# Optimization experiments

Measured on AMD Instinct MI355X. Metric: run time of the kernel, lower is better.

Reference implementation:

```python
import jax, jax.numpy as jnp
import numpy as np

N_E = 8192
E_DIM = 255  # spatial dim; full Lorentz dim = E_DIM + 1
BETA = 0.25
EPS = 1e-7


def _rand_lorentz(key, n, d):
    """Sample n points on the Lorentz manifold (curvature c=1), radii in [1,6]."""
    k1, k2 = jax.random.split(key)
    radii = jax.random.uniform(k1, (n, 1)) * 5.0 + 1.0
    t = jnp.cosh(radii)  # time component, >= cosh(1)
    dirs = jax.random.normal(k2, (n, d))
    dirs = dirs / jnp.linalg.norm(dirs, axis=-1, keepdims=True)
    s = dirs * jnp.sqrt(jnp.maximum(t ** 2 - 1.0, 1e-7))
    return jnp.concatenate([t, s], axis=-1)


def setup_inputs() -> dict:
    key = jax.random.key(0)
    k_u, k_cb = jax.random.split(key)
    B, H, W = 8, 32, 32
    u = _rand_lorentz(k_u, B * H * W, E_DIM).reshape(B, H, W, E_DIM + 1)
    codebook = _rand_lorentz(k_cb, N_E, E_DIM)
    return {"u_hyp": u, "codebook": codebook}


def reference(u_hyp, codebook):
    shape = u_hyp.shape
    d_full = E_DIM + 1
    u = u_hyp.reshape(-1, d_full)          # [N, D]
    n = u.shape[0]
    # Minkowski metric signs: (-, +, +, ..., +)
    signs = jnp.concatenate([-jnp.ones((1,), u.dtype), jnp.ones((E_DIM,), u.dtype)])

    # Lorentzian inner products with all codes: <u, c>_L = -u0*c0 + u_s . c_s
    K = (u * signs) @ codebook.T           # [N, n_e]
    dist = jnp.arccosh(jnp.maximum(-K, 1.0 + EPS))  # hyperbolic distance (c=1)
    idx = jnp.argmin(dist, axis=-1)        # [N]
    x_q = codebook[idx]                    # [N, D] gather

    def pdist(a, b):  # elementwise Lorentzian distance
        inner = jnp.sum(a * b * signs, axis=-1)
        return jnp.arccosh(jnp.maximum(-inner, 1.0 + EPS))

    sg = jax.lax.stop_gradient
    codebook_loss = pdist(sg(u), x_q).mean()
    commitment_loss = pdist(u, sg(x_q)).mean()
    loss = codebook_loss + BETA * commitment_loss

    # straight-through estimator
    z_q = (u + sg(x_q - u)).reshape(shape)

    counts = jnp.zeros((N_E,), u.dtype).at[idx].add(1.0)
    e_mean = counts / n
    entropy = -jnp.sum(e_mean * jnp.log(e_mean + 1e-10))
    perplexity = jnp.exp(entropy)
    diversity_loss = entropy
    return loss, z_q, perplexity, diversity_loss, e_mean
```

## Files before the change

### kernel.cpp

```cpp
#include <hip/hip_runtime.h>
#include <hip/hip_bf16.h>
#include <stdint.h>

#define N_PTS   8192
#define D       256
#define N_E     8192
#define BETA    0.25f
#define EPS_1   1.0000001f

typedef unsigned long long u64;
typedef __attribute__((ext_vector_type(8))) short bf16x8;
typedef __attribute__((ext_vector_type(8))) short short8;
typedef __attribute__((ext_vector_type(4))) float f32x4;

#define WS_KEYS    0
#define WS_COUNTS  (N_PTS * 8)
#define WS_LOSS    (WS_COUNTS + N_E * 4)
#define WS_RB_DONE (WS_LOSS + 16)
#define WS_GDONE   (WS_RB_DONE + 64 * 4)
#define WS_AHI     (1 << 20)
#define WS_ALO     (WS_AHI + N_PTS * D * 2)
#define WS_BHI     (WS_ALO + N_PTS * D * 2)
#define WS_BLO     (WS_BHI + N_E * D * 2)

__device__ __forceinline__ short f2bf(float x) {
    __hip_bfloat16 h = __float2bfloat16(x);
    return *reinterpret_cast<short*>(&h);
}
__device__ __forceinline__ float bf2f(short s) {
    __hip_bfloat16 h = *reinterpret_cast<__hip_bfloat16*>(&s);
    return __bfloat162float(h);
}

#define GLOAD16(gp, lp) __builtin_amdgcn_global_load_lds(                      \
    (const __attribute__((address_space(1))) void*)(gp),                       \
    (__attribute__((address_space(3))) void*)(lp), 16, 0, 0)

#define DPP_MIN(x, ctrl)                                                       \
    x = fminf(x, __int_as_float(__builtin_amdgcn_update_dpp(                   \
            __float_as_int(x), __float_as_int(x), (ctrl), 0xF, 0xF, true)))

__global__ __launch_bounds__(256) void k_prep(
    const float* __restrict__ u, const float* __restrict__ cb,
    short* __restrict__ Ahi, short* __restrict__ Alo,
    short* __restrict__ Bhi, short* __restrict__ Blo,
    u64* __restrict__ keys, float* __restrict__ counts,
    double* __restrict__ loss_sum, unsigned* __restrict__ rb_done,
    unsigned* __restrict__ gdone)
{
    const int tid = blockIdx.x * 256 + threadIdx.x;
    if (tid < N_E)   counts[tid] = 0.f;
    if (tid < N_PTS) keys[tid] = ~0ULL;
    if (tid == 0)    *loss_sum = 0.0;
    if (tid < 64)    rb_done[tid] = 0u;
    if (tid == 64)   *gdone = 0u;

    const int blk = tid >> 6;
    const int l   = tid & 63;
    const int s   = blk >> 3, c = blk & 7;
    const int p   = s * 16 + (l & 15);
    const int k   = c * 32 + (l >> 4) * 8;
    const size_t gin  = (size_t)p * D + k;
    const size_t gout = (size_t)tid * 8;

    float v[8];
    short8 h8, l8;

    *(float4*)&v[0] = *(const float4*)&u[gin];
    *(float4*)&v[4] = *(const float4*)&u[gin + 4];
    if (k == 0) v[0] = -v[0];
    #pragma unroll
    for (int j = 0; j < 8; ++j) {
        h8[j] = f2bf(v[j]);
        l8[j] = f2bf(v[j] - bf2f(h8[j]));
    }
    *(short8*)&Ahi[gout] = h8;
    *(short8*)&Alo[gout] = l8;

    *(float4*)&v[0] = *(const float4*)&cb[gin];
    *(float4*)&v[4] = *(const float4*)&cb[gin + 4];
    #pragma unroll
    for (int j = 0; j < 8; ++j) {
        h8[j] = f2bf(v[j]);
        l8[j] = f2bf(v[j] - bf2f(h8[j]));
    }
    *(short8*)&Bhi[gout] = h8;
    *(short8*)&Blo[gout] = l8;
}

#define BMM 128
#define BNN 128
#define NKS (D / 32)

__global__ __launch_bounds__(256, 4) void k_argmin_mfma(
    const short* __restrict__ Ahi, const short* __restrict__ Alo,
    const short* __restrict__ Bhi, const short* __restrict__ Blo,
    u64* __restrict__ keys,
    const float* __restrict__ u, const float* __restrict__ cb,
    float* __restrict__ out, float* __restrict__ counts,
    double* __restrict__ loss_sum, unsigned* __restrict__ rb_done,
    unsigned* __restrict__ gdone)
{
    __shared__ short sm[4][8 * 512];

    const int t   = threadIdx.x;
    const int w   = t >> 6;
    const int l   = t & 63;
    const int rb  = blockIdx.x >> 6;
    const int cbk = blockIdx.x & 63;
    const int r0  = rb * BMM, c0 = cbk * BNN;
    const int wr  = w >> 1, wc = w & 1;

    const short* gsrc = (w == 0) ? Ahi : (w == 1) ? Alo : (w == 2) ? Bhi : Blo;
    short* ldst = sm[w];
    const int s0 = ((w < 2) ? rb : cbk) * 8;

    f32x4 acc[4][4];
    #pragma unroll
    for (int i = 0; i < 4; ++i)
        #pragma unroll
        for (int j = 0; j < 4; ++j) acc[i][j] = (f32x4){0.f, 0.f, 0.f, 0.f};

    for (int kk = 0; kk < NKS; ++kk) {
        __syncthreads();
        #pragma unroll
        for (int i = 0; i < 8; ++i)
            GLOAD16(gsrc + (size_t)((s0 + i) * 8 + kk) * 512 + l * 8,
                    ldst + i * 512);
        __syncthreads();

        bf16x8 ah[4], al[4], bh[4], bl[4];
        #pragma unroll
        for (int f = 0; f < 4; ++f) {
            ah[f] = *(const bf16x8*)&sm[0][(wr * 4 + f) * 512 + l * 8];
            al[f] = *(const bf16x8*)&sm[1][(wr * 4 + f) * 512 + l * 8];
            bh[f] = *(const bf16x8*)&sm[2][(wc * 4 + f) * 512 + l * 8];
            bl[f] = *(const bf16x8*)&sm[3][(wc * 4 + f) * 512 + l * 8];
        }
        #pragma unroll
        for (int mf = 0; mf < 4; ++mf)
            #pragma unroll
            for (int nf = 0; nf < 4; ++nf) {
                acc[mf][nf] = __builtin_amdgcn_mfma_f32_16x16x32_bf16(
                    ah[mf], bh[nf], acc[mf][nf], 0, 0, 0);
                acc[mf][nf] = __builtin_amdgcn_mfma_f32_16x16x32_bf16(
                    ah[mf], bl[nf], acc[mf][nf], 0, 0, 0);
                acc[mf][nf] = __builtin_amdgcn_mfma_f32_16x16x32_bf16(
                    al[mf], bh[nf], acc[mf][nf], 0, 0, 0);
            }
    }

    const int g  = l >> 4;
    const int cc = l & 15;
    #pragma unroll
    for (int mf = 0; mf < 4; ++mf) {
        #pragma unroll
        for (int r = 0; r < 4; ++r) {
            float mm = fmaxf(-acc[mf][0][r], EPS_1);
            unsigned code = (unsigned)(c0 + wc * 64 + cc);
            #pragma unroll
            for (int nf = 1; nf < 4; ++nf) {
                float mv = fmaxf(-acc[mf][nf][r], EPS_1);
                if (mv < mm) { mm = mv; code = (unsigned)(c0 + wc * 64 + nf * 16 + cc); }
            }
            float mv = mm;
            DPP_MIN(mv, 0xB1);
            DPP_MIN(mv, 0x4E);
            DPP_MIN(mv, 0x141);
            DPP_MIN(mv, 0x140);
            if (mm == mv) {
                const int row = r0 + wr * 64 + mf * 16 + g * 4 + r;
                u64 key = ((u64)__float_as_uint(mm) << 32) | code;
                atomicMin(&keys[row], key);
            }
        }
    }

    int* sflagp = (int*)&sm[3][0];
    __syncthreads();
    if (t == 0)
        *sflagp = (atomicAdd(&rb_done[rb], 1u) == 63u) ? 1 : 0;
    __syncthreads();
    if (!*sflagp) return;

    u64* smk = (u64*)&sm[0][0];
    if (t < BMM)
        smk[t] = atomicMin(&keys[r0 + t], ~0ULL);
    __syncthreads();

    float* zq = out + 1;
    float fsum = 0.f;
    for (int rr = 0; rr < 32; ++rr) {
        const int lrow = w * 32 + rr;
        const int row  = r0 + lrow;
        const int idx  = (int)(unsigned)(smk[lrow] & 0xffffffffULL);
        float4 uv = *(const float4*)&u[(size_t)row * D + l * 4];
        float4 cv = *(const float4*)&cb[(size_t)idx * D + l * 4];
        if (l == 0) uv.x = -uv.x;
        float partial = uv.x * cv.x + uv.y * cv.y + uv.z * cv.z + uv.w * cv.w;
        *(float4*)&zq[(size_t)row * D + l * 4] = cv;
        #pragma unroll
        for (int s = 32; s >= 1; s >>= 1)
            partial += __shfl_xor(partial, s);
        if (l == 0) {
            fsum += acoshf(fmaxf(-partial, EPS_1));
            atomicAdd(&counts[idx], 1.f);
        }
    }
    if (l == 0) atomicAdd(loss_sum, (double)fsum);

    __syncthreads();
    if (t == 0)
        *sflagp = (atomicAdd(gdone, 1u) == 63u) ? 1 : 0;
    __syncthreads();
    if (!*sflagp) return;

    float* red = (float*)&sm[1][0];
    const int OFF_P = 1 + N_PTS * D;
    float ent = 0.f;
    for (int i = t; i < N_E; i += 256) {
        float cv_ = atomicAdd(&counts[i], 0.f);
        float e = cv_ * (1.0f / N_PTS);
        out[OFF_P + 2 + i] = e;
        ent -= e * logf(e + 1e-10f);
    }
    red[t] = ent;
    __syncthreads();
    for (int s = 128; s > 0; s >>= 1) {
        if (t < s) red[t] += red[t + s];
        __syncthreads();
    }
    if (t == 0) {
        float entropy = red[0];
        double ls = atomicAdd(loss_sum, 0.0);
        out[0]         = (1.0f + BETA) * (float)(ls / (double)N_PTS);
        out[OFF_P]     = expf(entropy);
        out[OFF_P + 1] = entropy;
    }
}

extern "C" void kernel_launch(void* const* d_in, const int* in_sizes, int n_in,
                              void* d_out, int out_size, void* d_ws, size_t ws_size,
                              hipStream_t stream)
{
    const float* u  = (const float*)d_in[0];
    const float* cb = (const float*)d_in[1];
    float* out = (float*)d_out;
    char* ws = (char*)d_ws;

    u64*      keys     = (u64*)(ws + WS_KEYS);
    float*    counts   = (float*)(ws + WS_COUNTS);
    double*   loss_sum = (double*)(ws + WS_LOSS);
    unsigned* rb_done  = (unsigned*)(ws + WS_RB_DONE);
    unsigned* gdone    = (unsigned*)(ws + WS_GDONE);
    short*    Ahi = (short*)(ws + WS_AHI);
    short*    Alo = (short*)(ws + WS_ALO);
    short*    Bhi = (short*)(ws + WS_BHI);
    short*    Blo = (short*)(ws + WS_BLO);

    k_prep<<<N_PTS * D / 8 / 256, 256, 0, stream>>>(
        u, cb, Ahi, Alo, Bhi, Blo, keys, counts, loss_sum, rb_done, gdone);
    k_argmin_mfma<<<(N_PTS / BMM) * (N_E / BNN), 256, 0, stream>>>(
        Ahi, Alo, Bhi, Blo, keys, u, cb, out, counts, loss_sum, rb_done, gdone);
}
```

Baseline: 185.9 us.

## Split gather/loss epilogue out of argmin kernel into separate wide kernel

Removes the last-block-per-row-band epilogue from the MFMA argmin kernel, which had only 64 blocks doing the gather, loss and count work serially over 32 rows per wave. A new k_gather kernel with one wave per row (2048 blocks) runs that work after the argmin kernel finishes, and the last block computes the entropy. This spreads the tail work across the whole GPU and drops the per-row-band counters, at the cost of an extra kernel launch and 2048 double atomics on the loss sum.

```diff
diff --git a/kernel.cpp b/kernel.cpp
--- a/kernel.cpp
+++ b/kernel.cpp
@@ -16,8 +16,7 @@
 #define WS_KEYS    0
 #define WS_COUNTS  (N_PTS * 8)
 #define WS_LOSS    (WS_COUNTS + N_E * 4)
-#define WS_RB_DONE (WS_LOSS + 16)
-#define WS_GDONE   (WS_RB_DONE + 64 * 4)
+#define WS_GDONE   (WS_LOSS + 16)
 #define WS_AHI     (1 << 20)
 #define WS_ALO     (WS_AHI + N_PTS * D * 2)
 #define WS_BHI     (WS_ALO + N_PTS * D * 2)
@@ -45,15 +44,12 @@
     short* __restrict__ Ahi, short* __restrict__ Alo,
     short* __restrict__ Bhi, short* __restrict__ Blo,
     u64* __restrict__ keys, float* __restrict__ counts,
-    double* __restrict__ loss_sum, unsigned* __restrict__ rb_done,
-    unsigned* __restrict__ gdone)
+    double* __restrict__ loss_sum, unsigned* __restrict__ gdone)
 {
     const int tid = blockIdx.x * 256 + threadIdx.x;
     if (tid < N_E)   counts[tid] = 0.f;
     if (tid < N_PTS) keys[tid] = ~0ULL;
-    if (tid == 0)    *loss_sum = 0.0;
-    if (tid < 64)    rb_done[tid] = 0u;
-    if (tid == 64)   *gdone = 0u;
+    if (tid == 0)  { *loss_sum = 0.0; *gdone = 0u; }
 
     const int blk = tid >> 6;
     const int l   = tid & 63;
@@ -95,11 +91,7 @@
 __global__ __launch_bounds__(256, 4) void k_argmin_mfma(
     const short* __restrict__ Ahi, const short* __restrict__ Alo,
     const short* __restrict__ Bhi, const short* __restrict__ Blo,
-    u64* __restrict__ keys,
-    const float* __restrict__ u, const float* __restrict__ cb,
-    float* __restrict__ out, float* __restrict__ counts,
-    double* __restrict__ loss_sum, unsigned* __restrict__ rb_done,
-    unsigned* __restrict__ gdone)
+    u64* __restrict__ keys)
 {
     __shared__ short sm[4][8 * 512];
 
@@ -175,47 +167,49 @@
             }
         }
     }
-
-    int* sflagp = (int*)&sm[3][0];
+}
+
+__global__ __launch_bounds__(256) void k_gather(
+    const float* __restrict__ u, const float* __restrict__ cb,
+    const u64* __restrict__ keys, float* __restrict__ out,
+    float* __restrict__ counts, double* __restrict__ loss_sum,
+    unsigned* __restrict__ gdone)
+{
+    __shared__ float sred[256];
+    __shared__ int   sflag;
+    const int t    = threadIdx.x;
+    const int w    = t >> 6;
+    const int row  = blockIdx.x * 4 + w;
+    const int lane = t & 63;
+    const u64 key  = keys[row];
+    const int idx  = (int)(unsigned)(key & 0xffffffffULL);
+
+    float* zq = out + 1;
+    float4 uv = *(const float4*)&u[(size_t)row * D + lane * 4];
+    float4 cv = *(const float4*)&cb[(size_t)idx * D + lane * 4];
+    if (lane == 0) uv.x = -uv.x;
+    float partial = uv.x * cv.x + uv.y * cv.y + uv.z * cv.z + uv.w * cv.w;
+    *(float4*)&zq[(size_t)row * D + lane * 4] = cv;
+
+    #pragma unroll
+    for (int s = 32; s >= 1; s >>= 1)
+        partial += __shfl_xor(partial, s);
+
+    if (lane == 0) {
+        float m = fmaxf(-partial, EPS_1);
+        sred[w] = acoshf(m);
+        atomicAdd(&counts[idx], 1.f);
+    }
     __syncthreads();
     if (t == 0)
-        *sflagp = (atomicAdd(&rb_done[rb], 1u) == 63u) ? 1 : 0;
-    __syncthreads();
-    if (!*sflagp) return;
-
-    u64* smk = (u64*)&sm[0][0];
-    if (t < BMM)
-        smk[t] = atomicMin(&keys[r0 + t], ~0ULL);
-    __syncthreads();
-
-    float* zq = out + 1;
-    float fsum = 0.f;
-    for (int rr = 0; rr < 32; ++rr) {
-        const int lrow = w * 32 + rr;
-        const int row  = r0 + lrow;
-        const int idx  = (int)(unsigned)(smk[lrow] & 0xffffffffULL);
-        float4 uv = *(const float4*)&u[(size_t)row * D + l * 4];
-        float4 cv = *(const float4*)&cb[(size_t)idx * D + l * 4];
-        if (l == 0) uv.x = -uv.x;
-        float partial = uv.x * cv.x + uv.y * cv.y + uv.z * cv.z + uv.w * cv.w;
-        *(float4*)&zq[(size_t)row * D + l * 4] = cv;
-        #pragma unroll
-        for (int s = 32; s >= 1; s >>= 1)
-            partial += __shfl_xor(partial, s);
-        if (l == 0) {
-            fsum += acoshf(fmaxf(-partial, EPS_1));
-            atomicAdd(&counts[idx], 1.f);
-        }
-    }
-    if (l == 0) atomicAdd(loss_sum, (double)fsum);
+        atomicAdd(loss_sum, (double)(sred[0] + sred[1] + sred[2] + sred[3]));
 
     __syncthreads();
     if (t == 0)
-        *sflagp = (atomicAdd(gdone, 1u) == 63u) ? 1 : 0;
-    __syncthreads();
-    if (!*sflagp) return;
-
-    float* red = (float*)&sm[1][0];
+        sflag = (atomicAdd(gdone, 1u) == (unsigned)(N_PTS / 4 - 1)) ? 1 : 0;
+    __syncthreads();
+    if (!sflag) return;
+
     const int OFF_P = 1 + N_PTS * D;
     float ent = 0.f;
     for (int i = t; i < N_E; i += 256) {
@@ -224,14 +218,14 @@
         out[OFF_P + 2 + i] = e;
         ent -= e * logf(e + 1e-10f);
     }
-    red[t] = ent;
+    sred[t] = ent;
     __syncthreads();
     for (int s = 128; s > 0; s >>= 1) {
-        if (t < s) red[t] += red[t + s];
+        if (t < s) sred[t] += sred[t + s];
         __syncthreads();
     }
     if (t == 0) {
-        float entropy = red[0];
+        float entropy = sred[0];
         double ls = atomicAdd(loss_sum, 0.0);
         out[0]         = (1.0f + BETA) * (float)(ls / (double)N_PTS);
         out[OFF_P]     = expf(entropy);
@@ -251,7 +245,6 @@
     u64*      keys     = (u64*)(ws + WS_KEYS);
     float*    counts   = (float*)(ws + WS_COUNTS);
     double*   loss_sum = (double*)(ws + WS_LOSS);
-    unsigned* rb_done  = (unsigned*)(ws + WS_RB_DONE);
     unsigned* gdone    = (unsigned*)(ws + WS_GDONE);
     short*    Ahi = (short*)(ws + WS_AHI);
     short*    Alo = (short*)(ws + WS_ALO);
@@ -259,7 +252,9 @@
     short*    Blo = (short*)(ws + WS_BLO);
 
     k_prep<<<N_PTS * D / 8 / 256, 256, 0, stream>>>(
-        u, cb, Ahi, Alo, Bhi, Blo, keys, counts, loss_sum, rb_done, gdone);
+        u, cb, Ahi, Alo, Bhi, Blo, keys, counts, loss_sum, gdone);
     k_argmin_mfma<<<(N_PTS / BMM) * (N_E / BNN), 256, 0, stream>>>(
-        Ahi, Alo, Bhi, Blo, keys, u, cb, out, counts, loss_sum, rb_done, gdone);
-}
+        Ahi, Alo, Bhi, Blo, keys);
+    k_gather<<<N_PTS / 4, 256, 0, stream>>>(
+        u, cb, keys, out, counts, loss_sum, gdone);
+}
```

New measurement: 175.4 us. 5.6% less time.
